# Kernel optimization log

Measured on AMD Instinct MI355X. Metric: run time of the kernel, lower is better.

The kernel has to match this reference:

```python
import jax, jax.numpy as jnp
import numpy as np

DIM = 1024
NUM_HEADS = 16
HEAD_DIM = DIM // NUM_HEADS
SCALE = HEAD_DIM ** -0.5


def setup_inputs() -> dict:
    key = jax.random.key(0)
    ks = jax.random.split(key, 5)
    B, N = 2, 2048
    x = jax.random.normal(ks[0], (B, N, DIM), dtype=jnp.float32)
    # nn.Linear weights: stored as [out, in]; we keep that convention.
    w_qkv = jax.random.normal(ks[1], (3 * DIM, DIM), dtype=jnp.float32) * (DIM ** -0.5)
    b_qkv = jax.random.normal(ks[2], (3 * DIM,), dtype=jnp.float32) * 0.02
    w_proj = jax.random.normal(ks[3], (DIM, DIM), dtype=jnp.float32) * (DIM ** -0.5)
    b_proj = jax.random.normal(ks[4], (DIM,), dtype=jnp.float32) * 0.02
    return {"x": x, "w_qkv": w_qkv, "b_qkv": b_qkv, "w_proj": w_proj, "b_proj": b_proj}


def reference(x, w_qkv, b_qkv, w_proj, b_proj):
    B, N, C = x.shape
    H, D = NUM_HEADS, HEAD_DIM
    qkv = x @ w_qkv.T + b_qkv                      # [B, N, 3C]
    qkv = qkv.reshape(B, N, 3, H, D)
    q = qkv[:, :, 0].transpose(0, 2, 1, 3)         # [B, H, N, D]
    k = qkv[:, :, 1].transpose(0, 2, 1, 3)
    v = qkv[:, :, 2].transpose(0, 2, 1, 3)
    attn = jnp.einsum("bhnd,bhmd->bhnm", q, k) * SCALE  # [B, H, N, N]
    attn = jax.nn.softmax(attn, axis=-1)
    out = jnp.einsum("bhnm,bhmd->bhnd", attn, v)   # [B, H, N, D]
    out = out.transpose(0, 2, 1, 3).reshape(B, N, C)
    return out @ w_proj.T + b_proj
```

## Files before the change

### kernel.cpp

```cpp
#include <hip/hip_runtime.h>
#include <math.h>

#define DIMC   1024
#define NHEADS 16
#define HDIM   64
#define BATCH  2
#define SEQ    2048

#define MTOT   (BATCH * SEQ)
#define QKVN   (3 * DIMC)
#define QKVSZ  ((size_t)BATCH * NHEADS * SEQ * HDIM)
#define HEADEL ((size_t)SEQ * HDIM)

#define QSCALE 0.18033688011112042f

typedef __attribute__((ext_vector_type(8))) short bf16x8;
typedef __attribute__((ext_vector_type(4))) short bf16x4;
typedef __attribute__((ext_vector_type(4))) float f32x4;

static __device__ inline short f2bf(float f) {
    union { float f; unsigned u; } v; v.f = f;
    unsigned r = v.u + 0x7fffu + ((v.u >> 16) & 1u);
    return (short)(r >> 16);
}

static __device__ inline unsigned cvt_pk_bf16(float lo, float hi) {
    unsigned r;
    asm("v_cvt_pk_bf16_f32 %0, %1, %2" : "=v"(r) : "v"(lo), "v"(hi));
    return r;
}

#if __has_builtin(__builtin_amdgcn_exp2f)
#define EXP2F(x) __builtin_amdgcn_exp2f(x)
#else
#define EXP2F(x) exp2f(x)
#endif

#define NXB  (MTOT * DIMC / 2048)
#define NWQB (QKVN * DIMC / 2048)
#define NWPB (DIMC * DIMC / 2048)

__global__ __launch_bounds__(256) void cast_all(
    const float* __restrict__ x,  const float* __restrict__ wq,
    const float* __restrict__ wp, short* __restrict__ xb,
    short* __restrict__ wqb, short* __restrict__ wpb)
{
    const float* in; short* out; int base;
    int bid = blockIdx.x;
    if (bid < NXB)              { in = x;  out = xb;  base = bid; }
    else if (bid < NXB + NWQB)  { in = wq; out = wqb; base = bid - NXB; }
    else                        { in = wp; out = wpb; base = bid - NXB - NWQB; }
    int i = (base * 256 + threadIdx.x) * 8;
    float4 a = *(const float4*)&in[i];
    float4 b = *(const float4*)&in[i + 4];
    bf16x8 o;
    o[0] = f2bf(a.x); o[1] = f2bf(a.y); o[2] = f2bf(a.z); o[3] = f2bf(a.w);
    o[4] = f2bf(b.x); o[5] = f2bf(b.y); o[6] = f2bf(b.z); o[7] = f2bf(b.w);
    *(bf16x8*)&out[i] = o;
}

__device__ __forceinline__ void gload16(const void* g, void* l) {
    __builtin_amdgcn_global_load_lds(
        (const __attribute__((address_space(1))) unsigned*)g,
        (__attribute__((address_space(3))) unsigned*)l, 16, 0, 0);
}

#define BAR() do { __builtin_amdgcn_s_barrier(); \
                   __builtin_amdgcn_sched_barrier(0); } while (0)
#define VWAIT8() asm volatile("s_waitcnt vmcnt(8)" ::: "memory")
#define VWAIT0() asm volatile("s_waitcnt vmcnt(0)" ::: "memory")

__device__ __forceinline__ void stage_panel(const short* __restrict__ src,
                                            int row0, int k0,
                                            short* dst, int tid)
{
#pragma unroll
    for (int u = 0; u < 2; ++u) {
        const int gidx = u * 512 + tid;
        const int rl   = gidx >> 3;
        const int cc   = gidx & 7;
        gload16(&src[(size_t)(row0 + rl) * 1024 + k0 + ((cc ^ (rl & 7)) << 3)],
                &dst[(size_t)gidx << 3]);
    }
}

template<int MH, int NH>
__device__ __forceinline__ void phase_compute(
    const short* As, const short* Bs,
    int wm, int wn, int lid, int quad, f32x4 (&acc)[8][4])
{
    bf16x8 af[4][2], bfr[2][2];
#pragma unroll
    for (int i2 = 0; i2 < 4; ++i2) {
        const int r = wm + (MH * 4 + i2) * 16 + lid;
#pragma unroll
        for (int kk = 0; kk < 2; ++kk)
            af[i2][kk] = *(const bf16x8*)
                &As[r * 64 + (((kk * 4 + quad) ^ (r & 7)) << 3)];
    }
#pragma unroll
    for (int j2 = 0; j2 < 2; ++j2) {
        const int rb = wn + (NH * 2 + j2) * 16 + lid;
#pragma unroll
        for (int kk = 0; kk < 2; ++kk)
            bfr[j2][kk] = *(const bf16x8*)
                &Bs[rb * 64 + (((kk * 4 + quad) ^ (rb & 7)) << 3)];
    }
    __builtin_amdgcn_s_setprio(1);
#pragma unroll
    for (int i2 = 0; i2 < 4; ++i2)
#pragma unroll
        for (int j2 = 0; j2 < 2; ++j2)
#pragma unroll
            for (int kk = 0; kk < 2; ++kk)
                acc[MH * 4 + i2][NH * 2 + j2] =
                    __builtin_amdgcn_mfma_f32_16x16x32_bf16(
                        af[i2][kk], bfr[j2][kk],
                        acc[MH * 4 + i2][NH * 2 + j2], 0, 0, 0);
    __builtin_amdgcn_s_setprio(0);
}

__global__ __launch_bounds__(512, 2) void qkv_mfma(
    const short* __restrict__ xb,
    const short* __restrict__ wb,
    const float* __restrict__ bias,
    short* __restrict__ qkvb)
{
    extern __shared__ short lds[];

    const int tid = threadIdx.x;
    const int T  = (blockIdx.x & 7) * 24 + (blockIdx.x >> 3);
    const int m0 = (T / 12) * 256;
    const int j0 = (T % 12) * 256;

    const int lane = tid & 63;
    const int w    = tid >> 6;
    const int quad = lane >> 4;
    const int lid  = lane & 15;
    const int wm = (w >> 2) * 128;
    const int wn = (w & 3) * 64;

    f32x4 acc[8][4];
#pragma unroll
    for (int i = 0; i < 8; ++i)
#pragma unroll
        for (int j = 0; j < 4; ++j) acc[i][j] = (f32x4){0.f, 0.f, 0.f, 0.f};

    stage_panel(xb, m0,       0, lds,                 tid);
    stage_panel(xb, m0 + 128, 0, lds + 8192,          tid);
    stage_panel(wb, j0,       0, lds + 32768,         tid);
    stage_panel(wb, j0 + 128, 0, lds + 32768 + 8192,  tid);

#pragma unroll 2
    for (int kt = 0; kt < 15; ++kt) {
        const int cb = (kt & 1) << 14;
        const int nb = (~kt & 1) << 14;
        const int k1 = (kt + 1) << 6;
        const short* Ac = lds + cb;
        const short* Bc = lds + 32768 + cb;
        short* An = lds + nb;
        short* Bn = lds + 32768 + nb;

        stage_panel(xb, m0,       k1, An,        tid);
        stage_panel(xb, m0 + 128, k1, An + 8192, tid);
        stage_panel(wb, j0,       k1, Bn,        tid);
        stage_panel(wb, j0 + 128, k1, Bn + 8192, tid);

        VWAIT8(); BAR();
        phase_compute<0, 0>(Ac, Bc, wm, wn, lid, quad, acc);
        BAR();
        phase_compute<0, 1>(Ac, Bc, wm, wn, lid, quad, acc);
        BAR();
        phase_compute<1, 0>(Ac, Bc, wm, wn, lid, quad, acc);
        BAR();
        phase_compute<1, 1>(Ac, Bc, wm, wn, lid, quad, acc);
        BAR();
    }
    {
        const short* Ac = lds + 16384;
        const short* Bc = lds + 32768 + 16384;
        VWAIT0(); BAR();
        phase_compute<0, 0>(Ac, Bc, wm, wn, lid, quad, acc);
        BAR();
        phase_compute<0, 1>(Ac, Bc, wm, wn, lid, quad, acc);
        BAR();
        phase_compute<1, 0>(Ac, Bc, wm, wn, lid, quad, acc);
        BAR();
        phase_compute<1, 1>(Ac, Bc, wm, wn, lid, quad, acc);
    }

    const int s = j0 >> 10;

    if (s == 0) {
#pragma unroll
        for (int jb = 0; jb < 4; ++jb) {
            const int jj = j0 + wn + jb * 16 + lid;
            const int hh = (jj & 1023) >> 6;
            const int dd = jj & 63;
            const float bv = bias[jj];
#pragma unroll
            for (int i = 0; i < 8; ++i)
#pragma unroll
                for (int r = 0; r < 4; ++r) {
                    const int mrow = m0 + wm + i * 16 + quad * 4 + r;
                    const int b_ = mrow >> 11, nn = mrow & 2047;
                    qkvb[((size_t)(b_ * NHEADS + hh) * SEQ + nn) * HDIM + dd] =
                        f2bf((acc[i][jb][r] + bv) * QSCALE);
                }
        }
    } else if (s == 1) {
#pragma unroll
        for (int jb = 0; jb < 4; ++jb) {
            const int jj = j0 + wn + jb * 16 + lid;
            const int hh = (jj & 1023) >> 6;
            const int dd = jj & 63;
            const int c2 = dd >> 5;
            const int qd = (dd >> 3) & 3;
            const int jo = dd & 7;
            const float bv = bias[jj];
#pragma unroll
            for (int i = 0; i < 8; ++i) {
                const int mrow0 = m0 + wm + i * 16;
                const int b_ = mrow0 >> 11;
                const int n0 = mrow0 & 2047;
                const int t32 = n0 >> 5;
                const int i16 = (n0 >> 4) & 1;
                const int c = quad & 1;
                const int lidb = (i16 * 2 + (quad >> 1)) * 4;
                size_t base = QKVSZ + (size_t)(b_ * NHEADS + hh) * HEADEL +
                              (size_t)(t32 * 4 + c2 * 2 + c) * 512 +
                              (qd * 16 + lidb) * 8 + jo;
#pragma unroll
                for (int r = 0; r < 4; ++r)
                    qkvb[base + r * 8] = f2bf(acc[i][jb][r] + bv);
            }
        }
    } else {
#pragma unroll
        for (int jb = 0; jb < 4; ++jb) {
            const int jj = j0 + wn + jb * 16 + lid;
            const int hh = (jj & 1023) >> 6;
            const int dd = jj & 63;
            const int fb = dd >> 4;
            const int dl = dd & 15;
            const float bv = bias[jj];
#pragma unroll
            for (int i = 0; i < 8; ++i) {
                const int mrow0 = m0 + wm + i * 16 + quad * 4;
                const int b_ = mrow0 >> 11, n0 = mrow0 & 2047;
                const int t32 = n0 >> 5;
                const int i16 = (n0 >> 4) & 1;
                const int quadpp = i16 * 2 + (quad >> 1);
                bf16x4 o;
#pragma unroll
                for (int r = 0; r < 4; ++r) o[r] = f2bf(acc[i][jb][r] + bv);
                *(bf16x4*)&qkvb[2 * QKVSZ + (size_t)(b_ * NHEADS + hh) * HEADEL +
                                (size_t)(t32 * 4 + fb) * 512 +
                                (quadpp * 16 + dl) * 8 + (quad & 1) * 4] = o;
            }
        }
    }
}

__global__ __launch_bounds__(256, 2) void attn_mfma(
    const short* __restrict__ qkvb,
    short* __restrict__ aob)
{
    __shared__ float Osm[2][4][4][4][64];
    __shared__ float Lsm[3][64];

    const int tid  = threadIdx.x;
    const int sp   = tid >> 6;
    const int lane = tid & 63;
    const int quad = lane >> 4;
    const int lid  = lane & 15;

    const int bid  = blockIdx.x;
    const int xcd  = bid & 7;
    const int slot = bid >> 3;
    const int pair = xcd * 4 + (slot >> 5);
    const int qblk = slot & 31;
    const int h = pair & 15;
    const int b = pair >> 4;
    const int qbase = qblk * 64;

    const short* Qh = qkvb + (size_t)(b * NHEADS + h) * HEADEL;
    const short* Kf = Qh + QKVSZ;
    const short* Vf = qkvb + 2 * QKVSZ + (size_t)(b * NHEADS + h) * HEADEL;

    bf16x8 bQ[4][2];
#pragma unroll
    for (int g = 0; g < 4; ++g)
#pragma unroll
        for (int c = 0; c < 2; ++c)
            bQ[g][c] = *(const bf16x8*)&Qh[(size_t)(qbase + g * 16 + lid) * HDIM +
                                           c * 32 + quad * 8];

    f32x4 O[4][4];
    f32x4 L[4];
#pragma unroll
    for (int g = 0; g < 4; ++g) {
        L[g] = (f32x4){0.f, 0.f, 0.f, 0.f};
#pragma unroll
        for (int fb = 0; fb < 4; ++fb) O[g][fb] = (f32x4){0.f, 0.f, 0.f, 0.f};
    }
    const bf16x8 ones8 = {(short)0x3F80, (short)0x3F80, (short)0x3F80, (short)0x3F80,
                          (short)0x3F80, (short)0x3F80, (short)0x3F80, (short)0x3F80};

#pragma unroll 2
    for (int cc = 0; cc < SEQ / 128; ++cc) {
        const int t = sp * (SEQ / 128) + cc;
        bf16x8 aK[2][2];
#pragma unroll
        for (int c = 0; c < 2; ++c)
#pragma unroll
            for (int c2 = 0; c2 < 2; ++c2)
                aK[c][c2] = *(const bf16x8*)&Kf[(size_t)(t * 4 + c2 * 2 + c) * 512 +
                                                lane * 8];
        bf16x8 aV[4];
#pragma unroll
        for (int fb = 0; fb < 4; ++fb)
            aV[fb] = *(const bf16x8*)&Vf[(size_t)(t * 4 + fb) * 512 + lane * 8];

#pragma unroll
        for (int g = 0; g < 4; ++g) {
            f32x4 s0 = (f32x4){0.f, 0.f, 0.f, 0.f};
            f32x4 s1 = (f32x4){0.f, 0.f, 0.f, 0.f};
            __builtin_amdgcn_s_setprio(1);
            s0 = __builtin_amdgcn_mfma_f32_16x16x32_bf16(aK[0][0], bQ[g][0], s0, 0, 0, 0);
            s1 = __builtin_amdgcn_mfma_f32_16x16x32_bf16(aK[1][0], bQ[g][0], s1, 0, 0, 0);
            s0 = __builtin_amdgcn_mfma_f32_16x16x32_bf16(aK[0][1], bQ[g][1], s0, 0, 0, 0);
            s1 = __builtin_amdgcn_mfma_f32_16x16x32_bf16(aK[1][1], bQ[g][1], s1, 0, 0, 0);
            __builtin_amdgcn_s_setprio(0);
            union { unsigned u[4]; bf16x8 v; } P;
            P.u[0] = cvt_pk_bf16(EXP2F(s0[0]), EXP2F(s0[1]));
            P.u[1] = cvt_pk_bf16(EXP2F(s0[2]), EXP2F(s0[3]));
            P.u[2] = cvt_pk_bf16(EXP2F(s1[0]), EXP2F(s1[1]));
            P.u[3] = cvt_pk_bf16(EXP2F(s1[2]), EXP2F(s1[3]));
            __builtin_amdgcn_s_setprio(1);
            L[g] = __builtin_amdgcn_mfma_f32_16x16x32_bf16(ones8, P.v, L[g], 0, 0, 0);
#pragma unroll
            for (int fb = 0; fb < 4; ++fb)
                O[g][fb] = __builtin_amdgcn_mfma_f32_16x16x32_bf16(
                    aV[fb], P.v, O[g][fb], 0, 0, 0);
            __builtin_amdgcn_s_setprio(0);
        }
    }

    if (sp != 0 && quad == 0)
#pragma unroll
        for (int g = 0; g < 4; ++g) Lsm[sp - 1][g * 16 + lid] = L[g][0];

    if (sp == 1 || sp == 3) {
        const int buf = sp >> 1;
#pragma unroll
        for (int g = 0; g < 4; ++g)
#pragma unroll
            for (int fb = 0; fb < 4; ++fb)
#pragma unroll
                for (int r = 0; r < 4; ++r)
                    Osm[buf][g][fb][r][lane] = O[g][fb][r];
    }
    __syncthreads();
    if (sp == 0 || sp == 2) {
        const int buf = sp >> 1;
#pragma unroll
        for (int g = 0; g < 4; ++g)
#pragma unroll
            for (int fb = 0; fb < 4; ++fb)
#pragma unroll
                for (int r = 0; r < 4; ++r)
                    O[g][fb][r] += Osm[buf][g][fb][r][lane];
    }
    __syncthreads();
    if (sp == 2) {
#pragma unroll
        for (int g = 0; g < 4; ++g)
#pragma unroll
            for (int fb = 0; fb < 4; ++fb)
#pragma unroll
                for (int r = 0; r < 4; ++r)
                    Osm[0][g][fb][r][lane] = O[g][fb][r];
    }
    __syncthreads();
    if (sp == 0) {
#pragma unroll
        for (int g = 0; g < 4; ++g) {
            const float lt = L[g][0] + Lsm[0][g * 16 + lid] +
                             Lsm[1][g * 16 + lid] + Lsm[2][g * 16 + lid];
            const float inv = 1.f / lt;
            const int n = qbase + g * 16 + lid;
            size_t base = ((size_t)(b * SEQ + n)) * DIMC + h * HDIM;
#pragma unroll
            for (int fb = 0; fb < 4; ++fb) {
                bf16x4 o;
#pragma unroll
                for (int r = 0; r < 4; ++r)
                    o[r] = f2bf((O[g][fb][r] + Osm[0][g][fb][r][lane]) * inv);
                *(bf16x4*)&aob[base + fb * 16 + quad * 4] = o;
            }
        }
    }
}

__global__ __launch_bounds__(256, 2) void proj_mfma(
    const short* __restrict__ ab,
    const short* __restrict__ wb,
    const float* __restrict__ bias,
    float* __restrict__ out)
{
    __shared__ __attribute__((aligned(16))) short Asm[2 * 64 * 32];
    __shared__ __attribute__((aligned(16))) short Bsm[2 * 128 * 32];

    const int tid = threadIdx.x;
    const int m0 = blockIdx.y * 64;
    const int j0 = blockIdx.x * 128;

    const int lane = tid & 63;
    const int w    = tid >> 6;
    const int quad = lane >> 4;
    const int lid  = lane & 15;
    const int wm = (w >> 1) * 32, wn = (w & 1) * 64;

    const int srow = lane >> 2;
    const int skc  = (lane & 3) * 8;

    f32x4 acc[2][4];
#pragma unroll
    for (int i = 0; i < 2; ++i)
#pragma unroll
        for (int j = 0; j < 4; ++j) acc[i][j] = (f32x4){0.f, 0.f, 0.f, 0.f};

    for (int k0 = 0; k0 < 1024; k0 += 64) {
        __syncthreads();
#pragma unroll
        for (int u = 0; u < 2; ++u) {
            const int combo = w * 2 + u;
            const int hh = combo >> 2, rb = combo & 3;
            const int row = rb * 16 + srow;
            gload16(&ab[(size_t)(m0 + row) * 1024 + k0 + hh * 32 + skc],
                    &Asm[hh * 2048 + row * 32 + skc]);
        }
#pragma unroll
        for (int u = 0; u < 4; ++u) {
            const int combo = w * 4 + u;
            const int hh = combo >> 3, rb = combo & 7;
            const int row = rb * 16 + srow;
            gload16(&wb[(size_t)(j0 + row) * 1024 + k0 + hh * 32 + skc],
                    &Bsm[hh * 4096 + row * 32 + skc]);
        }
        __syncthreads();

#pragma unroll
        for (int hh = 0; hh < 2; ++hh) {
            bf16x8 af[2], bfr[4];
#pragma unroll
            for (int i = 0; i < 2; ++i)
                af[i] = *(const bf16x8*)&Asm[hh * 2048 + (wm + i * 16 + lid) * 32 + quad * 8];
#pragma unroll
            for (int j = 0; j < 4; ++j)
                bfr[j] = *(const bf16x8*)&Bsm[hh * 4096 + (wn + j * 16 + lid) * 32 + quad * 8];
#pragma unroll
            for (int i = 0; i < 2; ++i)
#pragma unroll
                for (int j = 0; j < 4; ++j)
                    acc[i][j] = __builtin_amdgcn_mfma_f32_16x16x32_bf16(
                        af[i], bfr[j], acc[i][j], 0, 0, 0);
        }
    }

#pragma unroll
    for (int jb = 0; jb < 4; ++jb) {
        const int jj = j0 + wn + jb * 16 + lid;
        const float bv = bias[jj];
#pragma unroll
        for (int i = 0; i < 2; ++i)
#pragma unroll
            for (int r = 0; r < 4; ++r) {
                const int mrow = m0 + wm + i * 16 + quad * 4 + r;
                out[(size_t)mrow * DIMC + jj] = acc[i][jb][r] + bv;
            }
    }
}

extern "C" void kernel_launch(void* const* d_in, const int* in_sizes, int n_in,
                              void* d_out, int out_size, void* d_ws, size_t ws_size,
                              hipStream_t stream) {
    const float* x      = (const float*)d_in[0];
    const float* w_qkv  = (const float*)d_in[1];
    const float* b_qkv  = (const float*)d_in[2];
    const float* w_proj = (const float*)d_in[3];
    const float* b_proj = (const float*)d_in[4];
    float* out = (float*)d_out;

    short* qkvb   = (short*)d_ws;
    short* xb     = qkvb + 3 * QKVSZ;
    short* wqkvb  = xb + (size_t)MTOT * DIMC;
    short* wprojb = wqkvb + (size_t)QKVN * DIMC;
    short* aob    = wprojb + (size_t)DIMC * DIMC;

    hipFuncSetAttribute((const void*)qkv_mfma,
                        hipFuncAttributeMaxDynamicSharedMemorySize, 131072);

    cast_all<<<NXB + NWQB + NWPB, 256, 0, stream>>>(x, w_qkv, w_proj,
                                                    xb, wqkvb, wprojb);

    qkv_mfma<<<192, 512, 131072, stream>>>(xb, wqkvb, b_qkv, qkvb);

    attn_mfma<<<BATCH * NHEADS * (SEQ / 64), 256, 0, stream>>>(qkvb, aob);

    dim3 g3(DIMC / 128, MTOT / 64);
    proj_mfma<<<g3, 256, 0, stream>>>(aob, wprojb, b_proj, out);
}
```

Before: 177.0 us.

## Reuse LDS fragments across GEMM phases and zero-init attention scores from register

The QKV GEMM inner step now loads the A and B fragments once per half and reuses them across phases in a snake order (00, 01, 11, 10). Each of B's two halves is read from LDS once instead of twice, cutting LDS read traffic. In the attention loop, the score accumulators start from a zero vector held in a pinned register instead of being rematerialized for each group, saving the per-iteration zeroing moves. The cost is higher register pressure from keeping both B fragment sets live, plus extra barriers around the loads.

```diff
diff --git a/kernel.cpp b/kernel.cpp
--- a/kernel.cpp
+++ b/kernel.cpp
@@ -84,12 +84,23 @@
     }
 }
 
-template<int MH, int NH>
-__device__ __forceinline__ void phase_compute(
-    const short* As, const short* Bs,
-    int wm, int wn, int lid, int quad, f32x4 (&acc)[8][4])
-{
-    bf16x8 af[4][2], bfr[2][2];
+__device__ __forceinline__ void load_b(const short* Bs, int wn, int nh,
+                                       int lid, int quad, bf16x8 (&bfr)[2][2])
+{
+#pragma unroll
+    for (int j2 = 0; j2 < 2; ++j2) {
+        const int rb = wn + (nh * 2 + j2) * 16 + lid;
+#pragma unroll
+        for (int kk = 0; kk < 2; ++kk)
+            bfr[j2][kk] = *(const bf16x8*)
+                &Bs[rb * 64 + (((kk * 4 + quad) ^ (rb & 7)) << 3)];
+    }
+}
+
+template<int MH>
+__device__ __forceinline__ void load_a(const short* As, int wm,
+                                       int lid, int quad, bf16x8 (&af)[4][2])
+{
 #pragma unroll
     for (int i2 = 0; i2 < 4; ++i2) {
         const int r = wm + (MH * 4 + i2) * 16 + lid;
@@ -98,14 +109,13 @@
             af[i2][kk] = *(const bf16x8*)
                 &As[r * 64 + (((kk * 4 + quad) ^ (r & 7)) << 3)];
     }
-#pragma unroll
-    for (int j2 = 0; j2 < 2; ++j2) {
-        const int rb = wn + (NH * 2 + j2) * 16 + lid;
-#pragma unroll
-        for (int kk = 0; kk < 2; ++kk)
-            bfr[j2][kk] = *(const bf16x8*)
-                &Bs[rb * 64 + (((kk * 4 + quad) ^ (rb & 7)) << 3)];
-    }
+}
+
+template<int MH, int NH>
+__device__ __forceinline__ void mfma16(const bf16x8 (&af)[4][2],
+                                       const bf16x8 (&b)[2][2],
+                                       f32x4 (&acc)[8][4])
+{
     __builtin_amdgcn_s_setprio(1);
 #pragma unroll
     for (int i2 = 0; i2 < 4; ++i2)
@@ -115,7 +125,7 @@
             for (int kk = 0; kk < 2; ++kk)
                 acc[MH * 4 + i2][NH * 2 + j2] =
                     __builtin_amdgcn_mfma_f32_16x16x32_bf16(
-                        af[i2][kk], bfr[j2][kk],
+                        af[i2][kk], b[j2][kk],
                         acc[MH * 4 + i2][NH * 2 + j2], 0, 0, 0);
     __builtin_amdgcn_s_setprio(0);
 }
@@ -167,26 +177,43 @@
         stage_panel(wb, j0 + 128, k1, Bn + 8192, tid);
 
         VWAIT8(); BAR();
-        phase_compute<0, 0>(Ac, Bc, wm, wn, lid, quad, acc);
-        BAR();
-        phase_compute<0, 1>(Ac, Bc, wm, wn, lid, quad, acc);
-        BAR();
-        phase_compute<1, 0>(Ac, Bc, wm, wn, lid, quad, acc);
-        BAR();
-        phase_compute<1, 1>(Ac, Bc, wm, wn, lid, quad, acc);
+
+        bf16x8 af[4][2], b0[2][2], b1[2][2];
+        load_b(Bc, wn, 0, lid, quad, b0);
+        load_a<0>(Ac, wm, lid, quad, af);
+        BAR();
+        mfma16<0, 0>(af, b0, acc);
+        BAR();
+        load_b(Bc, wn, 1, lid, quad, b1);
+        BAR();
+        mfma16<0, 1>(af, b1, acc);
+        BAR();
+        load_a<1>(Ac, wm, lid, quad, af);
+        BAR();
+        mfma16<1, 1>(af, b1, acc);
+        BAR();
+        mfma16<1, 0>(af, b0, acc);
         BAR();
     }
     {
         const short* Ac = lds + 16384;
         const short* Bc = lds + 32768 + 16384;
         VWAIT0(); BAR();
-        phase_compute<0, 0>(Ac, Bc, wm, wn, lid, quad, acc);
-        BAR();
-        phase_compute<0, 1>(Ac, Bc, wm, wn, lid, quad, acc);
-        BAR();
-        phase_compute<1, 0>(Ac, Bc, wm, wn, lid, quad, acc);
-        BAR();
-        phase_compute<1, 1>(Ac, Bc, wm, wn, lid, quad, acc);
+        bf16x8 af[4][2], b0[2][2], b1[2][2];
+        load_b(Bc, wn, 0, lid, quad, b0);
+        load_a<0>(Ac, wm, lid, quad, af);
+        BAR();
+        mfma16<0, 0>(af, b0, acc);
+        BAR();
+        load_b(Bc, wn, 1, lid, quad, b1);
+        BAR();
+        mfma16<0, 1>(af, b1, acc);
+        BAR();
+        load_a<1>(Ac, wm, lid, quad, af);
+        BAR();
+        mfma16<1, 1>(af, b1, acc);
+        BAR();
+        mfma16<1, 0>(af, b0, acc);
     }
 
     const int s = j0 >> 10;
@@ -306,6 +333,8 @@
     }
     const bf16x8 ones8 = {(short)0x3F80, (short)0x3F80, (short)0x3F80, (short)0x3F80,
                           (short)0x3F80, (short)0x3F80, (short)0x3F80, (short)0x3F80};
+    f32x4 Z = (f32x4){0.f, 0.f, 0.f, 0.f};
+    asm volatile("" : "+v"(Z));
 
 #pragma unroll 2
     for (int cc = 0; cc < SEQ / 128; ++cc) {
@@ -324,11 +353,10 @@
 
 #pragma unroll
         for (int g = 0; g < 4; ++g) {
-            f32x4 s0 = (f32x4){0.f, 0.f, 0.f, 0.f};
-            f32x4 s1 = (f32x4){0.f, 0.f, 0.f, 0.f};
+            f32x4 s0, s1;
             __builtin_amdgcn_s_setprio(1);
-            s0 = __builtin_amdgcn_mfma_f32_16x16x32_bf16(aK[0][0], bQ[g][0], s0, 0, 0, 0);
-            s1 = __builtin_amdgcn_mfma_f32_16x16x32_bf16(aK[1][0], bQ[g][0], s1, 0, 0, 0);
+            s0 = __builtin_amdgcn_mfma_f32_16x16x32_bf16(aK[0][0], bQ[g][0], Z, 0, 0, 0);
+            s1 = __builtin_amdgcn_mfma_f32_16x16x32_bf16(aK[1][0], bQ[g][0], Z, 0, 0, 0);
             s0 = __builtin_amdgcn_mfma_f32_16x16x32_bf16(aK[0][1], bQ[g][1], s0, 0, 0, 0);
             s1 = __builtin_amdgcn_mfma_f32_16x16x32_bf16(aK[1][1], bQ[g][1], s1, 0, 0, 0);
             __builtin_amdgcn_s_setprio(0);
```

New measurement: 179.9 us. Within noise of the previous version (+1.7%).
